# Performance work log

Measured on AMD Instinct MI355X. Metric: run time of the kernel, lower is better.

## Reference

```python
import jax, jax.numpy as jnp
import numpy as np

BS, NPOINT, N, C = 2, 128, 8192, 128
NUM_CLASS, HEAD_BINS, K = 3, 12, 64
MLP1, MLP2, IOU_H = 128, 256, 128
EPS_BN = 1e-5


def setup_inputs():
    key = jax.random.key(0)
    ks = jax.random.split(key, 16)
    rn = lambda k, s, sc=1.0: jax.random.normal(k, s, jnp.float32) * sc
    return {
        'original_xyz': rn(ks[0], (BS, N, 3), 10.0),
        'original_feature': rn(ks[1], (BS, C, N)),
        'candidate_xyz': rn(ks[2], (BS, NPOINT, 3), 10.0),
        'pred_cls': rn(ks[3], (BS, NPOINT, NUM_CLASS)),
        'pred_offsets': rn(ks[4], (BS, NPOINT, 6)),
        'pred_angle_cls': rn(ks[5], (BS, NPOINT, HEAD_BINS)),
        'pred_angle_res': rn(ks[6], (BS, NPOINT, HEAD_BINS), 0.1),
        'w_mlp1': rn(ks[7], (MLP1, C + 3), 0.05), 'b_mlp1': jnp.zeros((MLP1,), jnp.float32),
        'w_mlp2': rn(ks[8], (MLP2, MLP1), 0.05), 'b_mlp2': jnp.zeros((MLP2,), jnp.float32),
        'w_iou0': rn(ks[9], (IOU_H, MLP2), 0.05), 'b_iou0': jnp.zeros((IOU_H,), jnp.float32),
        'g_iou0': jnp.ones((IOU_H,), jnp.float32), 'be_iou0': jnp.zeros((IOU_H,), jnp.float32),
        'w_iou1': rn(ks[10], (IOU_H, IOU_H), 0.05), 'b_iou1': jnp.zeros((IOU_H,), jnp.float32),
        'g_iou1': jnp.ones((IOU_H,), jnp.float32), 'be_iou1': jnp.zeros((IOU_H,), jnp.float32),
        'w_iou2': rn(ks[11], (1, IOU_H), 0.05), 'b_iou2': jnp.zeros((1,), jnp.float32),
    }


def _bn1d(x, g, b):
    # training-mode BatchNorm1d over (batch, length)
    m = jnp.mean(x, (0, 2), keepdims=True)
    v = jnp.var(x, (0, 2), keepdims=True)
    return (x - m) / jnp.sqrt(v + EPS_BN) * g[None, :, None] + b[None, :, None]


def _forward(original_xyz, original_feature, candidate_xyz, pred_cls, pred_offsets,
             pred_angle_cls, pred_angle_res, w_mlp1, b_mlp1, w_mlp2, b_mlp2,
             w_iou0, b_iou0, g_iou0, be_iou0, w_iou1, b_iou1, g_iou1, be_iou1,
             w_iou2, b_iou2):
    sg = jax.lax.stop_gradient
    original_xyz = sg(original_xyz)
    original_feature = sg(original_feature)
    bs, npoint = candidate_xyz.shape[0], candidate_xyz.shape[1]
    # --- decode_prediction (detached in original) ---
    acls = jnp.argmax(pred_angle_cls, -1)                              # [bs,np]
    ares = jnp.take_along_axis(pred_angle_res, acls[..., None], -1)[..., 0]
    apc = 2.0 * np.pi / HEAD_BINS
    angle = acls.astype(jnp.float32) * apc + ares
    heading = sg(jnp.where(angle > np.pi, angle - 2.0 * np.pi, angle))
    center = sg(candidate_xyz + pred_offsets[:, :, :3])
    lwh = sg(jnp.maximum(pred_offsets[:, :, 3:6] * 2.0, 0.1))
    # --- 4x4x4 grid scaled by box dims ---
    gs = jnp.linspace(-1.0, 1.0, 4)
    gx, gy, gz = jnp.meshgrid(gs, gs, gs, indexing='ij')
    grid = jnp.stack([gx.ravel(), gy.ravel(), gz.ravel()], -1)          # [64,3]
    whole_grid = grid[None, None] * lwh[:, :, None, :]                  # [bs,np,64,3]
    # --- rotation about z ---
    c, s = jnp.cos(heading), jnp.sin(heading)
    z = jnp.zeros_like(c); o = jnp.ones_like(c)
    R = jnp.stack([jnp.stack([c, s, z], -1),
                   jnp.stack([-s, c, z], -1),
                   jnp.stack([z, z, o], -1)], -2)                        # [bs,np,3,3]
    rel = jnp.einsum('bpkc,bpcd->bpkd', whole_grid, R)                   # [bs,np,64,3]
    corners = (rel + center[:, :, None, :]).reshape(bs, npoint * K, 3)   # [bs,M,3]
    # --- three_nn: 3 nearest original points per corner ---
    d2 = (jnp.sum(corners ** 2, -1)[:, :, None]
          + jnp.sum(original_xyz ** 2, -1)[:, None, :]
          - 2.0 * jnp.einsum('bmc,bnc->bmn', corners, original_xyz))     # [bs,M,N]
    _, idx = jax.lax.top_k(-d2, 3)                                       # [bs,M,3]
    nn_xyz = jax.vmap(lambda pts, i: pts[i])(original_xyz, idx)          # [bs,M,3,3]
    dist = jnp.sqrt(jnp.sum((nn_xyz - corners[:, :, None, :]) ** 2, -1)) # [bs,M,3]
    w = 1.0 / (dist + 1e-8)
    w = w / jnp.sum(w, -1, keepdims=True)
    nn_feat = jax.vmap(lambda f, i: f[:, i])(original_feature, idx)      # [bs,C,M,3]
    interp = jnp.sum(nn_feat * w[:, None], -1).reshape(bs, -1, npoint, K)
    feat = jnp.concatenate([rel.transpose(0, 3, 1, 2), interp], 1)       # [bs,C+3,np,K]
    # --- CGE shared MLP (1x1 conv + relu) ---
    h = jax.nn.relu(jnp.einsum('oc,bcpk->bopk', w_mlp1, feat) + b_mlp1[None, :, None, None])
    h = jax.nn.relu(jnp.einsum('oc,bcpk->bopk', w_mlp2, h) + b_mlp2[None, :, None, None])
    h = jnp.max(h, -1)                                                   # [bs,256,np]
    # --- IoU head ---
    h = jax.nn.relu(_bn1d(jnp.einsum('oc,bcp->bop', w_iou0, h) + b_iou0[None, :, None], g_iou0, be_iou0))
    h = jax.nn.relu(_bn1d(jnp.einsum('oc,bcp->bop', w_iou1, h) + b_iou1[None, :, None], g_iou1, be_iou1))
    return jnp.einsum('oc,bcp->bop', w_iou2, h) + b_iou2[None, :, None]  # [bs,1,np]


def reference(original_xyz, original_feature, candidate_xyz, pred_cls, pred_offsets,
              pred_angle_cls, pred_angle_res, w_mlp1, b_mlp1, w_mlp2, b_mlp2,
              w_iou0, b_iou0, g_iou0, be_iou0, w_iou1, b_iou1, g_iou1, be_iou1,
              w_iou2, b_iou2):
    return _forward(original_xyz, original_feature, candidate_xyz, pred_cls, pred_offsets,
                    pred_angle_cls, pred_angle_res, w_mlp1, b_mlp1, w_mlp2, b_mlp2,
                    w_iou0, b_iou0, g_iou0, be_iou0, w_iou1, b_iou1, g_iou1, be_iou1,
                    w_iou2, b_iou2)
```

## Files before the change

kernel.cpp:

```cpp
#include <hip/hip_runtime.h>
#include <math.h>

#define BSZ 2
#define NPOINT 128
#define NPTS 8192
#define CH_F 128
#define HEAD_BINS 12
#define KCOR 64
#define MTOT (NPOINT*KCOR)
#define NCH 16
#define CHUNK (NPTS/NCH)
#define FEAT_C 131
#define MLP2_C 256

#define OFF_CORNERS 0u
#define OFF_REL     196608u
#define OFF_PD      393216u
#define OFF_PIX     3538944u
#define OFF_FEATT   6684672u
#define OFF_W1T     15073280u
#define OFF_W2T     15140352u
#define OFF_XYZP    15271424u
#define OFF_H2      15533568u
#define OFF_X0      15795712u
#define OFF_X1      15926784u
#define OFF_BN0     16057856u
#define OFF_BN1     16058880u

__global__ __launch_bounds__(256) void k_prep(const float* __restrict__ cand, const float* __restrict__ offs,
                        const float* __restrict__ angc, const float* __restrict__ angr,
                        const float* __restrict__ w1, const float* __restrict__ w2,
                        const float* __restrict__ of, const float* __restrict__ xyz,
                        float* __restrict__ corners, float* __restrict__ rel,
                        float* __restrict__ w1t, float* __restrict__ w2t,
                        float* __restrict__ ft, float4* __restrict__ xyzp)
{
    __shared__ float tile[128][17];
    __shared__ float sr[4*KCOR*3];
    __shared__ float sc_[4*KCOR*3];
    int bid = blockIdx.x;
    int t = threadIdx.x;
    if (bid < 64) {
        int b = bid >> 5, p0 = (bid & 31) * 4;
        int lb = t >> 6, k = t & 63;
        int bp = b*NPOINT + p0 + lb;
        const float* ac = angc + bp*HEAD_BINS;
        int best = 0; float bv = ac[0];
        #pragma unroll
        for (int j = 1; j < HEAD_BINS; ++j) { float v = ac[j]; if (v > bv) { bv = v; best = j; } }
        float ares = angr[bp*HEAD_BINS + best];
        float angle = (float)best * 0.52359877559829882f + ares;
        float heading = (angle > 3.14159265358979323f) ? (angle - 6.28318530717958647f) : angle;
        float cx = cand[bp*3+0] + offs[bp*6+0];
        float cy = cand[bp*3+1] + offs[bp*6+1];
        float cz = cand[bp*3+2] + offs[bp*6+2];
        float dl = fmaxf(offs[bp*6+3]*2.0f, 0.1f);
        float dw = fmaxf(offs[bp*6+4]*2.0f, 0.1f);
        float dh = fmaxf(offs[bp*6+5]*2.0f, 0.1f);
        float chd = cosf(heading), shd = sinf(heading);
        int ix = (k>>4)&3, iy = (k>>2)&3, iz = k&3;
        float gx = (ix==3) ? 1.0f : (-1.0f + (2.0f/3.0f)*(float)ix);
        float gy = (iy==3) ? 1.0f : (-1.0f + (2.0f/3.0f)*(float)iy);
        float gz = (iz==3) ? 1.0f : (-1.0f + (2.0f/3.0f)*(float)iz);
        float wx = gx*dl, wy = gy*dw, wz = gz*dh;
        float rx = wx*chd - wy*shd;
        float ry = wx*shd + wy*chd;
        int si = (lb*KCOR + k)*3;
        sr[si+0] = rx;      sr[si+1] = ry;      sr[si+2] = wz;
        sc_[si+0] = rx+cx;  sc_[si+1] = ry+cy;  sc_[si+2] = wz+cz;
        __syncthreads();
        size_t base = ((size_t)b*MTOT + (size_t)p0*KCOR)*3;
        if (t < 192) {
            ((float4*)(rel + base))[t]     = ((const float4*)sr)[t];
            ((float4*)(corners + base))[t] = ((const float4*)sc_)[t];
        }
    } else if (bid < 80) {
        int i0 = (bid-64)*256 + t;
        for (int i = i0; i < FEAT_C*128; i += 16*256) { int o = i & 127, c = i >> 7; w1t[i] = w1[o*FEAT_C + c]; }
        for (int i = i0; i < 128*256;    i += 16*256) { int o = i & 255, c = i >> 8; w2t[i] = w2[o*128 + c]; }
    } else if (bid < 144) {
        int i = (bid-80)*256 + t;
        const float* s = xyz + (size_t)i*3;
        float x = s[0], y = s[1], z = s[2];
        xyzp[i] = make_float4(x, y, z, (x*x + y*y) + z*z);
    } else {
        int bi = bid - 144;
        int b = bi >> 9;
        int n0 = (bi & 511) * 16;
        #pragma unroll
        for (int it = 0; it < 2; ++it) {
            int id = it*256 + t;
            int c = id >> 2, q = id & 3;
            float4 v = *(const float4*)(of + ((size_t)(b*CH_F + c))*NPTS + n0 + q*4);
            tile[c][q*4+0] = v.x; tile[c][q*4+1] = v.y; tile[c][q*4+2] = v.z; tile[c][q*4+3] = v.w;
        }
        __syncthreads();
        #pragma unroll
        for (int it = 0; it < 2; ++it) {
            int id = it*256 + t;
            int n = id >> 5, cq = id & 31;
            float4 o;
            o.x = tile[cq*4+0][n]; o.y = tile[cq*4+1][n]; o.z = tile[cq*4+2][n]; o.w = tile[cq*4+3][n];
            *(float4*)(ft + ((size_t)b*NPTS + n0 + n)*CH_F + cq*4) = o;
        }
    }
}

__global__ __launch_bounds__(256) void k_three_nn(const float4* __restrict__ xyzp,
        const float* __restrict__ corners, float* __restrict__ pd, int* __restrict__ pix)
{
    __shared__ float4 pts[CHUNK];
    int mb = blockIdx.x;
    int ch = blockIdx.y;
    int b  = blockIdx.z;
    int t = threadIdx.x;

    if (t < 128) {
        const float4* s4 = xyzp + ((size_t)b*NPTS + (size_t)ch*CHUNK);
        #pragma unroll
        for (int j = 0; j < 4; ++j) pts[t*4+j] = s4[t*4+j];
    }
    __syncthreads();

    int m = mb*256 + t;
    const float* cp = corners + ((size_t)b*MTOT + m)*3;
    float cx = cp[0], cy = cp[1], cz = cp[2];
    float sc = (cx*cx + cy*cy) + cz*cz;
    float s0 = 3.4e38f, s1 = 3.4e38f, s2 = 3.4e38f;
    int i0 = 0, i1 = 0, i2 = 0;
    #pragma unroll 8
    for (int n = 0; n < CHUNK; ++n) {
        float4 P = pts[n];
        float dot = fmaf(cz, P.z, fmaf(cy, P.y, cx*P.x));
        float d2 = (sc + P.w) - 2.0f*dot;
        bool l0 = d2 < s0, l1 = d2 < s1, l2 = d2 < s2;
        i2 = l1 ? i1 : (l2 ? n : i2);
        i1 = l0 ? i0 : (l1 ? n : i1);
        i0 = l0 ? n : i0;
        s2 = __builtin_amdgcn_fmed3f(d2, s1, s2);
        s1 = __builtin_amdgcn_fmed3f(d2, s0, s1);
        s0 = fminf(d2, s0);
    }
    int nb = ch*CHUNK;
    size_t ob = (((size_t)b*MTOT + m)*NCH + ch)*3;
    pd[ob+0] = s0; pd[ob+1] = s1; pd[ob+2] = s2;
    pix[ob+0] = nb+i0; pix[ob+1] = nb+i1; pix[ob+2] = nb+i2;
}

__global__ __launch_bounds__(512) void k_mlp(const float* __restrict__ xyz, const float* __restrict__ corners,
        const float* __restrict__ pd, const int* __restrict__ pix,
        const float* __restrict__ featT, const float* __restrict__ rel,
        const float* __restrict__ w1t, const float* __restrict__ b1,
        const float* __restrict__ w2t, const float* __restrict__ b2,
        float* __restrict__ h2)
{
    __shared__ float lds[FEAT_C*64];
    __shared__ float swt[3][64];
    __shared__ int   sidx[3][64];
    int blk = blockIdx.x; int b = blk >> 7, p = blk & 127;
    int t = threadIdx.x;
    int g0 = b*MTOT + p*KCOR;

    if (t < 64) {
        int g = g0 + t;
        float s0=3.4e38f, s1=3.4e38f, s2=3.4e38f;
        int i0=0x7fffffff, i1=0x7fffffff, i2=0x7fffffff;
        size_t base = (size_t)g*(NCH*3);
        for (int k = 0; k < NCH*3; ++k) {
            float d = pd[base+k]; int id = pix[base+k];
            bool lt0 = (d < s0) || (d == s0 && id < i0);
            bool lt1 = (d < s1) || (d == s1 && id < i1);
            bool lt2 = (d < s2) || (d == s2 && id < i2);
            s2 = lt1 ? s1 : (lt2 ? d  : s2); i2 = lt1 ? i1 : (lt2 ? id : i2);
            s1 = lt0 ? s0 : (lt1 ? d  : s1); i1 = lt0 ? i0 : (lt1 ? id : i1);
            s0 = lt0 ? d  : s0;              i0 = lt0 ? id : i0;
        }
        float cx = corners[(size_t)g*3+0], cy = corners[(size_t)g*3+1], cz = corners[(size_t)g*3+2];
        int ii[3] = {i0, i1, i2};
        float w[3];
        #pragma unroll
        for (int j = 0; j < 3; ++j) {
            const float* pp = xyz + ((size_t)b*NPTS + ii[j])*3;
            float dx = pp[0]-cx, dy = pp[1]-cy, dz = pp[2]-cz;
            float dist = sqrtf((dx*dx + dy*dy) + dz*dz);
            w[j] = 1.0f/(dist + 1e-8f);
        }
        float wsum = (w[0]+w[1])+w[2];
        #pragma unroll
        for (int j = 0; j < 3; ++j) { sidx[j][t] = ii[j]; swt[j][t] = w[j]/wsum; }
    } else if (t < 256) {
        int u = t - 64;
        lds[(u % 3)*64 + (u / 3)] = rel[(size_t)g0*3 + u];
    }
    __syncthreads();

    const float4* fb = (const float4*)(featT + (size_t)b*NPTS*CH_F);
    #pragma unroll
    for (int it = 0; it < 4; ++it) {
        int idx = it*512 + t;
        int cq = idx >> 6, m = idx & 63;
        int j0 = sidx[0][m], j1 = sidx[1][m], j2 = sidx[2][m];
        float w0 = swt[0][m], w1 = swt[1][m], w2 = swt[2][m];
        float4 f0 = fb[(size_t)j0*32 + cq];
        float4 f1 = fb[(size_t)j1*32 + cq];
        float4 f2 = fb[(size_t)j2*32 + cq];
        float4 v;
        v.x = (f0.x*w0 + f1.x*w1) + f2.x*w2;
        v.y = (f0.y*w0 + f1.y*w1) + f2.y*w2;
        v.z = (f0.z*w0 + f1.z*w1) + f2.z*w2;
        v.w = (f0.w*w0 + f1.w*w1) + f2.w*w2;
        int c0 = 3 + cq*4;
        lds[(c0+0)*64+m] = v.x; lds[(c0+1)*64+m] = v.y;
        lds[(c0+2)*64+m] = v.z; lds[(c0+3)*64+m] = v.w;
    }
    __syncthreads();

    int og = t >> 4, mg = t & 15;
    float acc[4][4];
    #pragma unroll
    for (int i = 0; i < 4; ++i) { float bb = b1[og*4+i];
        #pragma unroll
        for (int j = 0; j < 4; ++j) acc[i][j] = bb; }
    #pragma unroll 4
    for (int c = 0; c < FEAT_C; ++c) {
        float4 wv = *(const float4*)(w1t + c*128 + og*4);
        float4 f0 = *(const float4*)(&lds[c*64 + mg*4]);
        float fv[4] = {f0.x,f0.y,f0.z,f0.w};
        float wa[4] = {wv.x,wv.y,wv.z,wv.w};
        #pragma unroll
        for (int i = 0; i < 4; ++i)
            #pragma unroll
            for (int j = 0; j < 4; ++j)
                acc[i][j] = fmaf(wa[i], fv[j], acc[i][j]);
    }
    __syncthreads();
    #pragma unroll
    for (int i = 0; i < 4; ++i) {
        float4 r0 = make_float4(fmaxf(acc[i][0],0.f), fmaxf(acc[i][1],0.f), fmaxf(acc[i][2],0.f), fmaxf(acc[i][3],0.f));
        *(float4*)(&lds[(og*4+i)*64 + mg*4]) = r0;
    }
    __syncthreads();

    int og2 = t >> 3, mg2 = t & 7;
    float a2[4][8];
    #pragma unroll
    for (int i = 0; i < 4; ++i) { float bb = b2[og2*4+i];
        #pragma unroll
        for (int j = 0; j < 8; ++j) a2[i][j] = bb; }
    #pragma unroll 2
    for (int c = 0; c < 128; ++c) {
        float4 wv = *(const float4*)(w2t + c*MLP2_C + og2*4);
        float4 f0 = *(const float4*)(&lds[c*64 + mg2*8]);
        float4 f1 = *(const float4*)(&lds[c*64 + mg2*8 + 4]);
        float fv[8] = {f0.x,f0.y,f0.z,f0.w,f1.x,f1.y,f1.z,f1.w};
        float wa[4] = {wv.x,wv.y,wv.z,wv.w};
        #pragma unroll
        for (int i = 0; i < 4; ++i)
            #pragma unroll
            for (int j = 0; j < 8; ++j)
                a2[i][j] = fmaf(wa[i], fv[j], a2[i][j]);
    }
    float mx[4];
    #pragma unroll
    for (int i = 0; i < 4; ++i) {
        float m0 = a2[i][0];
        #pragma unroll
        for (int j = 1; j < 8; ++j) m0 = fmaxf(m0, a2[i][j]);
        mx[i] = fmaxf(m0, 0.0f);
    }
    #pragma unroll
    for (int off = 1; off < 8; off <<= 1)
        #pragma unroll
        for (int i = 0; i < 4; ++i)
            mx[i] = fmaxf(mx[i], __shfl_xor(mx[i], off, 64));
    if (mg2 == 0)
        *(float4*)(&h2[((size_t)b*NPOINT + p)*MLP2_C + og2*4]) = make_float4(mx[0],mx[1],mx[2],mx[3]);
}

__global__ __launch_bounds__(256) void k_head0(const float* __restrict__ h2, const float* __restrict__ w0,
                        const float* __restrict__ b0, const float* __restrict__ g0,
                        const float* __restrict__ be0,
                        float* __restrict__ x0, float* __restrict__ bn0)
{
    __shared__ float ssum[256], ssq[256];
    int o = blockIdx.x;
    int t = threadIdx.x;
    int b = t >> 7, p = t & 127;
    const float4* hb = (const float4*)(h2 + ((size_t)b*NPOINT + p)*MLP2_C);
    const float4* wr = (const float4*)(w0 + (size_t)o*MLP2_C);
    float acc = b0[o];
    #pragma unroll 8
    for (int cq = 0; cq < 64; ++cq) {
        float4 h = hb[cq], w = wr[cq];
        acc = fmaf(h.x, w.x, acc); acc = fmaf(h.y, w.y, acc);
        acc = fmaf(h.z, w.z, acc); acc = fmaf(h.w, w.w, acc);
    }
    x0[((size_t)b*NPOINT + p)*128 + o] = acc;
    ssum[t] = acc; ssq[t] = acc*acc;
    __syncthreads();
    if (t < 128) { ssum[t] += ssum[t+128]; ssq[t] += ssq[t+128]; }
    __syncthreads();
    if (t < 64) {
        float s = ssum[t] + ssum[t+64];
        float q = ssq[t] + ssq[t+64];
        #pragma unroll
        for (int off = 32; off >= 1; off >>= 1) {
            s += __shfl_down(s, off, 64);
            q += __shfl_down(q, off, 64);
        }
        if (t == 0) {
            float mean = s * (1.0f/256.0f);
            float var  = q * (1.0f/256.0f) - mean*mean;
            if (var < 0.f) var = 0.f;
            float scale = g0[o] / sqrtf(var + 1e-5f);
            bn0[o]       = scale;
            bn0[128 + o] = be0[o] - mean*scale;
        }
    }
}

__global__ __launch_bounds__(256) void k_head1(const float* __restrict__ x0, const float* __restrict__ bn0,
                        const float* __restrict__ w1, const float* __restrict__ b1,
                        const float* __restrict__ g1, const float* __restrict__ be1,
                        float* __restrict__ x1, float* __restrict__ bn1)
{
    __shared__ float ssum[256], ssq[256];
    int o = blockIdx.x;
    int t = threadIdx.x;
    int b = t >> 7, p = t & 127;
    const float4* xb = (const float4*)(x0 + ((size_t)b*NPOINT + p)*128);
    const float4* wr = (const float4*)(w1 + (size_t)o*128);
    float acc = b1[o];
    #pragma unroll 8
    for (int cq = 0; cq < 32; ++cq) {
        float4 xv = xb[cq], wv = wr[cq];
        float4 sc = *(const float4*)(bn0 + cq*4);
        float4 sh = *(const float4*)(bn0 + 128 + cq*4);
        acc = fmaf(wv.x, fmaxf(fmaf(xv.x, sc.x, sh.x), 0.0f), acc);
        acc = fmaf(wv.y, fmaxf(fmaf(xv.y, sc.y, sh.y), 0.0f), acc);
        acc = fmaf(wv.z, fmaxf(fmaf(xv.z, sc.z, sh.z), 0.0f), acc);
        acc = fmaf(wv.w, fmaxf(fmaf(xv.w, sc.w, sh.w), 0.0f), acc);
    }
    x1[((size_t)b*NPOINT + p)*128 + o] = acc;
    ssum[t] = acc; ssq[t] = acc*acc;
    __syncthreads();
    if (t < 128) { ssum[t] += ssum[t+128]; ssq[t] += ssq[t+128]; }
    __syncthreads();
    if (t < 64) {
        float s = ssum[t] + ssum[t+64];
        float q = ssq[t] + ssq[t+64];
        #pragma unroll
        for (int off = 32; off >= 1; off >>= 1) {
            s += __shfl_down(s, off, 64);
            q += __shfl_down(q, off, 64);
        }
        if (t == 0) {
            float mean = s * (1.0f/256.0f);
            float var  = q * (1.0f/256.0f) - mean*mean;
            if (var < 0.f) var = 0.f;
            float scale = g1[o] / sqrtf(var + 1e-5f);
            bn1[o]       = scale;
            bn1[128 + o] = be1[o] - mean*scale;
        }
    }
}

__global__ void k_final(const float* __restrict__ x1, const float* __restrict__ bn1,
                        const float* __restrict__ w2, const float* __restrict__ b2,
                        float* __restrict__ out)
{
    int t = threadIdx.x;
    int b = t >> 7, p = t & 127;
    const float4* xb = (const float4*)(x1 + ((size_t)b*NPOINT + p)*128);
    float acc = b2[0];
    #pragma unroll 8
    for (int cq = 0; cq < 32; ++cq) {
        float4 xv = xb[cq];
        float4 wv = *(const float4*)(w2 + cq*4);
        float4 sc = *(const float4*)(bn1 + cq*4);
        float4 sh = *(const float4*)(bn1 + 128 + cq*4);
        acc = fmaf(wv.x, fmaxf(fmaf(xv.x, sc.x, sh.x), 0.0f), acc);
        acc = fmaf(wv.y, fmaxf(fmaf(xv.y, sc.y, sh.y), 0.0f), acc);
        acc = fmaf(wv.z, fmaxf(fmaf(xv.z, sc.z, sh.z), 0.0f), acc);
        acc = fmaf(wv.w, fmaxf(fmaf(xv.w, sc.w, sh.w), 0.0f), acc);
    }
    out[b*NPOINT + p] = acc;
}

extern "C" void kernel_launch(void* const* d_in, const int* in_sizes, int n_in,
                              void* d_out, int out_size, void* d_ws, size_t ws_size,
                              hipStream_t stream)
{
    const float* xyz   = (const float*)d_in[0];
    const float* ofeat = (const float*)d_in[1];
    const float* cand  = (const float*)d_in[2];
    const float* offs  = (const float*)d_in[4];
    const float* angc  = (const float*)d_in[5];
    const float* angr  = (const float*)d_in[6];
    const float* w1    = (const float*)d_in[7];
    const float* b1    = (const float*)d_in[8];
    const float* w2    = (const float*)d_in[9];
    const float* b2    = (const float*)d_in[10];
    const float* wi0   = (const float*)d_in[11];
    const float* bi0   = (const float*)d_in[12];
    const float* gi0   = (const float*)d_in[13];
    const float* bei0  = (const float*)d_in[14];
    const float* wi1   = (const float*)d_in[15];
    const float* bi1   = (const float*)d_in[16];
    const float* gi1   = (const float*)d_in[17];
    const float* bei1  = (const float*)d_in[18];
    const float* wi2   = (const float*)d_in[19];
    const float* bi2   = (const float*)d_in[20];

    char* ws = (char*)d_ws;
    float*  corners = (float*)(ws + OFF_CORNERS);
    float*  rel     = (float*)(ws + OFF_REL);
    float*  pd      = (float*)(ws + OFF_PD);
    int*    pix     = (int*)  (ws + OFF_PIX);
    float*  featT   = (float*)(ws + OFF_FEATT);
    float*  w1t     = (float*)(ws + OFF_W1T);
    float*  w2t     = (float*)(ws + OFF_W2T);
    float4* xyzp    = (float4*)(ws + OFF_XYZP);
    float*  h2      = (float*)(ws + OFF_H2);
    float*  x0      = (float*)(ws + OFF_X0);
    float*  x1      = (float*)(ws + OFF_X1);
    float*  bn0     = (float*)(ws + OFF_BN0);
    float*  bn1     = (float*)(ws + OFF_BN1);

    k_prep     <<<1168, 256, 0, stream>>>(cand, offs, angc, angr, w1, w2, ofeat, xyz,
                                          corners, rel, w1t, w2t, featT, xyzp);
    k_three_nn <<<dim3(32,16,2), 256, 0, stream>>>(xyzp, corners, pd, pix);
    k_mlp      <<<256, 512, 0, stream>>>(xyz, corners, pd, pix, featT, rel,
                                         w1t, b1, w2t, b2, h2);
    k_head0    <<<128, 256, 0, stream>>>(h2, wi0, bi0, gi0, bei0, x0, bn0);
    k_head1    <<<128, 256, 0, stream>>>(x0, bn0, wi1, bi1, gi1, bei1, x1, bn1);
    k_final    <<<1, 256, 0, stream>>>(x1, bn1, wi2, bi2, (float*)d_out);
}
```

Baseline: 232.1 us.

## Prune three-NN candidates per proposal with a triangle-inequality radius bound

Replaces the brute-force three-NN over all 8192 points for every corner with a per-proposal pruning pass. Each block finds the third-nearest distance from the box center, derives a radius bound from the box diagonal, and compacts the points inside that radius into shared memory. Each corner then scans only this candidate list. The final top-3 merge and the interpolation weights move out of k_mlp into this kernel, which removes the per-chunk partial buffers. The cost is that the candidate list is built twice (once per half block), atomics are used for compaction, and correctness depends on the bound and on the corners lying within the box extent.

Result: no change. 230.3 us (-0.8%).

```diff
diff --git a/kernel.cpp b/kernel.cpp
--- a/kernel.cpp
+++ b/kernel.cpp
@@ -8,15 +8,13 @@
 #define HEAD_BINS 12
 #define KCOR 64
 #define MTOT (NPOINT*KCOR)
-#define NCH 16
-#define CHUNK (NPTS/NCH)
 #define FEAT_C 131
 #define MLP2_C 256
 
 #define OFF_CORNERS 0u
 #define OFF_REL     196608u
-#define OFF_PD      393216u
-#define OFF_PIX     3538944u
+#define OFF_IDX3    393216u
+#define OFF_W3      589824u
 #define OFF_FEATT   6684672u
 #define OFF_W1T     15073280u
 #define OFF_W2T     15140352u
@@ -106,49 +104,167 @@
     }
 }
 
-__global__ __launch_bounds__(256) void k_three_nn(const float4* __restrict__ xyzp,
-        const float* __restrict__ corners, float* __restrict__ pd, int* __restrict__ pix)
-{
-    __shared__ float4 pts[CHUNK];
-    int mb = blockIdx.x;
-    int ch = blockIdx.y;
-    int b  = blockIdx.z;
+__global__ __launch_bounds__(512) void k_three_nn(const float4* __restrict__ xyzp,
+        const float* __restrict__ cand, const float* __restrict__ offs,
+        const float* __restrict__ corners,
+        int* __restrict__ idx3, float* __restrict__ w3)
+{
+    __shared__ int   lidx[NPTS];
+    __shared__ float red[1752];
+    __shared__ float pms[512*3];
+    __shared__ int   pmi[512*3];
+    __shared__ int   s_cnt;
+    __shared__ float s_T;
+
+    int bid = blockIdx.x;
+    int b    = bid >> 8;
+    int p    = (bid >> 1) & 127;
+    int half = bid & 1;
     int t = threadIdx.x;
-
-    if (t < 128) {
-        const float4* s4 = xyzp + ((size_t)b*NPTS + (size_t)ch*CHUNK);
-        #pragma unroll
-        for (int j = 0; j < 4; ++j) pts[t*4+j] = s4[t*4+j];
-    }
-    __syncthreads();
-
-    int m = mb*256 + t;
-    const float* cp = corners + ((size_t)b*MTOT + m)*3;
-    float cx = cp[0], cy = cp[1], cz = cp[2];
-    float sc = (cx*cx + cy*cy) + cz*cz;
+    int bp = b*NPOINT + p;
+
+    float cx = cand[bp*3+0] + offs[bp*6+0];
+    float cy = cand[bp*3+1] + offs[bp*6+1];
+    float cz = cand[bp*3+2] + offs[bp*6+2];
+    float dl = fmaxf(offs[bp*6+3]*2.0f, 0.1f);
+    float dw = fmaxf(offs[bp*6+4]*2.0f, 0.1f);
+    float dh = fmaxf(offs[bp*6+5]*2.0f, 0.1f);
+    float H  = sqrtf((dl*dl + dw*dw) + dh*dh);
+    float scc = (cx*cx + cy*cy) + cz*cz;
+
+    const float4* xb = xyzp + (size_t)b*NPTS;
+
+    float d2c[16];
+    float a0 = 3.4e38f, a1 = 3.4e38f, a2 = 3.4e38f;
+    #pragma unroll
+    for (int i = 0; i < 16; ++i) {
+        float4 P = xb[i*512 + t];
+        float dot = fmaf(cz, P.z, fmaf(cy, P.y, cx*P.x));
+        float d2 = (scc + P.w) - 2.0f*dot;
+        d2c[i] = d2;
+        a2 = __builtin_amdgcn_fmed3f(d2, a1, a2);
+        a1 = __builtin_amdgcn_fmed3f(d2, a0, a1);
+        a0 = fminf(d2, a0);
+    }
+    red[t*3+0] = a0; red[t*3+1] = a1; red[t*3+2] = a2;
+    if (t == 0) s_cnt = 0;
+    __syncthreads();
+    if (t < 64) {
+        float m0 = 3.4e38f, m1 = 3.4e38f, m2 = 3.4e38f;
+        for (int s = t*8; s < t*8+8; ++s) {
+            #pragma unroll
+            for (int j = 0; j < 3; ++j) {
+                float v = red[s*3+j];
+                m2 = __builtin_amdgcn_fmed3f(v, m1, m2);
+                m1 = __builtin_amdgcn_fmed3f(v, m0, m1);
+                m0 = fminf(v, m0);
+            }
+        }
+        red[1536 + t*3+0] = m0; red[1536 + t*3+1] = m1; red[1536 + t*3+2] = m2;
+    }
+    __syncthreads();
+    if (t < 8) {
+        float m0 = 3.4e38f, m1 = 3.4e38f, m2 = 3.4e38f;
+        for (int s = t*8; s < t*8+8; ++s) {
+            #pragma unroll
+            for (int j = 0; j < 3; ++j) {
+                float v = red[1536 + s*3+j];
+                m2 = __builtin_amdgcn_fmed3f(v, m1, m2);
+                m1 = __builtin_amdgcn_fmed3f(v, m0, m1);
+                m0 = fminf(v, m0);
+            }
+        }
+        red[1728 + t*3+0] = m0; red[1728 + t*3+1] = m1; red[1728 + t*3+2] = m2;
+    }
+    __syncthreads();
+    if (t == 0) {
+        float m0 = 3.4e38f, m1 = 3.4e38f, m2 = 3.4e38f;
+        for (int s = 0; s < 8; ++s) {
+            #pragma unroll
+            for (int j = 0; j < 3; ++j) {
+                float v = red[1728 + s*3+j];
+                m2 = __builtin_amdgcn_fmed3f(v, m1, m2);
+                m1 = __builtin_amdgcn_fmed3f(v, m0, m1);
+                m0 = fminf(v, m0);
+            }
+        }
+        float r3 = sqrtf(fmaxf(m2, 0.0f));
+        float rad = r3 + 2.0f*H;
+        s_T = rad*rad*1.0002f + 0.25f;
+    }
+    __syncthreads();
+
+    float T = s_T;
+    #pragma unroll
+    for (int i = 0; i < 16; ++i) {
+        if (d2c[i] <= T) {
+            int pos = atomicAdd(&s_cnt, 1);
+            lidx[pos] = i*512 + t;
+        }
+    }
+    __syncthreads();
+    int C = s_cnt;
+
+    int ck  = half*32 + (t >> 4);
+    int sub = t & 15;
+    size_t crow = (size_t)b*MTOT + p*KCOR + ck;
+    float ox = corners[crow*3+0], oy = corners[crow*3+1], oz = corners[crow*3+2];
+    float so = (ox*ox + oy*oy) + oz*oz;
     float s0 = 3.4e38f, s1 = 3.4e38f, s2 = 3.4e38f;
-    int i0 = 0, i1 = 0, i2 = 0;
-    #pragma unroll 8
-    for (int n = 0; n < CHUNK; ++n) {
-        float4 P = pts[n];
-        float dot = fmaf(cz, P.z, fmaf(cy, P.y, cx*P.x));
-        float d2 = (sc + P.w) - 2.0f*dot;
-        bool l0 = d2 < s0, l1 = d2 < s1, l2 = d2 < s2;
-        i2 = l1 ? i1 : (l2 ? n : i2);
-        i1 = l0 ? i0 : (l1 ? n : i1);
-        i0 = l0 ? n : i0;
-        s2 = __builtin_amdgcn_fmed3f(d2, s1, s2);
-        s1 = __builtin_amdgcn_fmed3f(d2, s0, s1);
-        s0 = fminf(d2, s0);
-    }
-    int nb = ch*CHUNK;
-    size_t ob = (((size_t)b*MTOT + m)*NCH + ch)*3;
-    pd[ob+0] = s0; pd[ob+1] = s1; pd[ob+2] = s2;
-    pix[ob+0] = nb+i0; pix[ob+1] = nb+i1; pix[ob+2] = nb+i2;
-}
-
-__global__ __launch_bounds__(512) void k_mlp(const float* __restrict__ xyz, const float* __restrict__ corners,
-        const float* __restrict__ pd, const int* __restrict__ pix,
+    int i0 = 0x7fffffff, i1 = 0x7fffffff, i2 = 0x7fffffff;
+    for (int j = sub; j < C; j += 16) {
+        int idx = lidx[j];
+        float4 P = xb[idx];
+        float dot = fmaf(oz, P.z, fmaf(oy, P.y, ox*P.x));
+        float d2 = (so + P.w) - 2.0f*dot;
+        bool lt0 = (d2 < s0) || (d2 == s0 && idx < i0);
+        bool lt1 = (d2 < s1) || (d2 == s1 && idx < i1);
+        bool lt2 = (d2 < s2) || (d2 == s2 && idx < i2);
+        s2 = lt1 ? s1 : (lt2 ? d2  : s2); i2 = lt1 ? i1 : (lt2 ? idx : i2);
+        s1 = lt0 ? s0 : (lt1 ? d2  : s1); i1 = lt0 ? i0 : (lt1 ? idx : i1);
+        s0 = lt0 ? d2 : s0;               i0 = lt0 ? idx : i0;
+    }
+    pms[t*3+0] = s0; pms[t*3+1] = s1; pms[t*3+2] = s2;
+    pmi[t*3+0] = i0; pmi[t*3+1] = i1; pmi[t*3+2] = i2;
+    __syncthreads();
+
+    if (t < 32) {
+        float f0 = 3.4e38f, f1 = 3.4e38f, f2 = 3.4e38f;
+        int   j0 = 0x7fffffff, j1 = 0x7fffffff, j2 = 0x7fffffff;
+        for (int tt = t*16; tt < t*16+16; ++tt) {
+            #pragma unroll
+            for (int j = 0; j < 3; ++j) {
+                float d = pms[tt*3+j]; int id = pmi[tt*3+j];
+                bool lt0 = (d < f0) || (d == f0 && id < j0);
+                bool lt1 = (d < f1) || (d == f1 && id < j1);
+                bool lt2 = (d < f2) || (d == f2 && id < j2);
+                f2 = lt1 ? f1 : (lt2 ? d  : f2); j2 = lt1 ? j1 : (lt2 ? id : j2);
+                f1 = lt0 ? f0 : (lt1 ? d  : f1); j1 = lt0 ? j0 : (lt1 ? id : j1);
+                f0 = lt0 ? d  : f0;              j0 = lt0 ? id : j0;
+            }
+        }
+        int ckf = half*32 + t;
+        size_t row = (size_t)b*MTOT + p*KCOR + ckf;
+        float qx = corners[row*3+0], qy = corners[row*3+1], qz = corners[row*3+2];
+        int ii[3] = {j0, j1, j2};
+        float w[3];
+        #pragma unroll
+        for (int j = 0; j < 3; ++j) {
+            float4 P = xb[ii[j]];
+            float dx = P.x - qx, dy = P.y - qy, dz = P.z - qz;
+            float dist = sqrtf((dx*dx + dy*dy) + dz*dz);
+            w[j] = 1.0f/(dist + 1e-8f);
+        }
+        float wsum = (w[0]+w[1])+w[2];
+        #pragma unroll
+        for (int j = 0; j < 3; ++j) {
+            idx3[row*3+j] = ii[j];
+            w3[row*3+j]   = w[j]/wsum;
+        }
+    }
+}
+
+__global__ __launch_bounds__(512) void k_mlp(const int* __restrict__ idx3, const float* __restrict__ w3,
         const float* __restrict__ featT, const float* __restrict__ rel,
         const float* __restrict__ w1t, const float* __restrict__ b1,
         const float* __restrict__ w2t, const float* __restrict__ b2,
@@ -162,32 +278,9 @@
     int g0 = b*MTOT + p*KCOR;
 
     if (t < 64) {
-        int g = g0 + t;
-        float s0=3.4e38f, s1=3.4e38f, s2=3.4e38f;
-        int i0=0x7fffffff, i1=0x7fffffff, i2=0x7fffffff;
-        size_t base = (size_t)g*(NCH*3);
-        for (int k = 0; k < NCH*3; ++k) {
-            float d = pd[base+k]; int id = pix[base+k];
-            bool lt0 = (d < s0) || (d == s0 && id < i0);
-            bool lt1 = (d < s1) || (d == s1 && id < i1);
-            bool lt2 = (d < s2) || (d == s2 && id < i2);
-            s2 = lt1 ? s1 : (lt2 ? d  : s2); i2 = lt1 ? i1 : (lt2 ? id : i2);
-            s1 = lt0 ? s0 : (lt1 ? d  : s1); i1 = lt0 ? i0 : (lt1 ? id : i1);
-            s0 = lt0 ? d  : s0;              i0 = lt0 ? id : i0;
-        }
-        float cx = corners[(size_t)g*3+0], cy = corners[(size_t)g*3+1], cz = corners[(size_t)g*3+2];
-        int ii[3] = {i0, i1, i2};
-        float w[3];
-        #pragma unroll
-        for (int j = 0; j < 3; ++j) {
-            const float* pp = xyz + ((size_t)b*NPTS + ii[j])*3;
-            float dx = pp[0]-cx, dy = pp[1]-cy, dz = pp[2]-cz;
-            float dist = sqrtf((dx*dx + dy*dy) + dz*dz);
-            w[j] = 1.0f/(dist + 1e-8f);
-        }
-        float wsum = (w[0]+w[1])+w[2];
-        #pragma unroll
-        for (int j = 0; j < 3; ++j) { sidx[j][t] = ii[j]; swt[j][t] = w[j]/wsum; }
+        size_t row = (size_t)(g0 + t)*3;
+        #pragma unroll
+        for (int j = 0; j < 3; ++j) { sidx[j][t] = idx3[row+j]; swt[j][t] = w3[row+j]; }
     } else if (t < 256) {
         int u = t - 64;
         lds[(u % 3)*64 + (u / 3)] = rel[(size_t)g0*3 + u];
@@ -415,8 +508,8 @@
     char* ws = (char*)d_ws;
     float*  corners = (float*)(ws + OFF_CORNERS);
     float*  rel     = (float*)(ws + OFF_REL);
-    float*  pd      = (float*)(ws + OFF_PD);
-    int*    pix     = (int*)  (ws + OFF_PIX);
+    int*    idx3    = (int*)  (ws + OFF_IDX3);
+    float*  w3      = (float*)(ws + OFF_W3);
     float*  featT   = (float*)(ws + OFF_FEATT);
     float*  w1t     = (float*)(ws + OFF_W1T);
     float*  w2t     = (float*)(ws + OFF_W2T);
@@ -429,8 +522,8 @@
 
     k_prep     <<<1168, 256, 0, stream>>>(cand, offs, angc, angr, w1, w2, ofeat, xyz,
                                           corners, rel, w1t, w2t, featT, xyzp);
-    k_three_nn <<<dim3(32,16,2), 256, 0, stream>>>(xyzp, corners, pd, pix);
-    k_mlp      <<<256, 512, 0, stream>>>(xyz, corners, pd, pix, featT, rel,
+    k_three_nn <<<512, 512, 0, stream>>>(xyzp, cand, offs, corners, idx3, w3);
+    k_mlp      <<<256, 512, 0, stream>>>(idx3, w3, featT, rel,
                                          w1t, b1, w2t, b2, h2);
     k_head0    <<<128, 256, 0, stream>>>(h2, wi0, bi0, gi0, bei0, x0, bn0);
     k_head1    <<<128, 256, 0, stream>>>(x0, bn0, wi1, bi1, gi1, bei1, x1, bn1);
```
